# Optimization experiments

Hardware: AMD Instinct MI355X
Metric: run time of the kernel (lower is better)

Reference implementation:

```python
import jax, jax.numpy as jnp
import numpy as np

H, E, V = 1024, 8, 32000
B, S = 2, 2048
RANK, ALPHA = 4, 1.0
LORA_SCALE = ALPHA / RANK
TOP_K = 2
C1, DEC = 4096, 256
CACHE_SIZES = np.array([C1 - i * DEC for i in range(E)])  # [4096,...,2304]
CMAX = int(CACHE_SIZES.max())
H2 = H // 2  # pyramid compression ratio 0.5


def setup_inputs() -> dict:
    key = jax.random.key(0)
    ks = jax.random.split(key, 24)
    n = lambda k, shape, s=1.0: jax.random.normal(k, shape, dtype=jnp.float32) * s
    w = 1.0 / np.sqrt(H)
    inp = {
        "x": n(ks[0], (B, S, H)),
        "query": n(ks[1], (B, S, H)),
        "cache_values": n(ks[2], (E, CMAX, H)),
        "cache_importance": jax.random.uniform(ks[3], (E, CMAX), dtype=jnp.float32),
        "Wr": n(ks[4], (H, E), w),
        "Wexp": n(ks[5], (E, H, H), w),
        "bexp": jnp.zeros((E, H), jnp.float32),
        "Aexp": n(ks[6], (E, H, RANK), w),
        "Bexp": n(ks[7], (E, RANK, H), w),
        "Wq": n(ks[8], (H, H), w),
        "bq": jnp.zeros((H,), jnp.float32),
        "Wk": n(ks[9], (H, H), w),
        "bk": jnp.zeros((H,), jnp.float32),
        "Aq": n(ks[10], (H, RANK), w),
        "Bq": n(ks[11], (RANK, H), w),
        "Ak": n(ks[12], (H, RANK), w),
        "Bk": n(ks[13], (RANK, H), w),
        "Wd": n(ks[14], (H, H2), w),
        "Wu": n(ks[15], (H2, H), 1.0 / np.sqrt(H2)),
        "Av": n(ks[16], (E, H, RANK), w),
        "Bv": n(ks[17], (E, RANK, H), w),
        "Wv": n(ks[18], (H, V), w),
        "bv": jnp.zeros((V,), jnp.float32),
    }
    # compressor weights are per-expert in the original (one per KVCache)
    inp["Wd"] = n(ks[19], (E, H, H2), w)
    inp["Wu"] = n(ks[20], (E, H2, H), 1.0 / np.sqrt(H2))
    return inp


def reference(x, query, cache_values, cache_importance, Wr, Wexp, bexp, Aexp, Bexp,
              Wq, bq, Wk, bk, Aq, Bq, Ak, Bk, Wd, Wu, Av, Bv, Wv, bv):
    # ---- AdaptiveRouter: softmax gate, top-2, renormalize, scatter to dense ----
    gate = jax.nn.softmax(jnp.einsum("bsh,he->bse", x, Wr), axis=-1)       # [B,S,E]
    topv, topi = jax.lax.top_k(gate, TOP_K)                                 # [B,S,K]
    topv = topv / jnp.sum(topv, axis=-1, keepdims=True)
    rw = jnp.sum(jax.nn.one_hot(topi, E, dtype=x.dtype) * topv[..., None], axis=-2)  # [B,S,E]

    # ---- compute_token_importance: LoRA-augmented q/k projections + attention ----
    q = query @ Wq + bq + LORA_SCALE * ((query @ Aq) @ Bq)                  # [B,S,H]
    k = x @ Wk + bk + LORA_SCALE * ((x @ Ak) @ Bk)                          # [B,S,H]
    att = jax.nn.softmax(jnp.einsum("bqh,bkh->bqk", q, k) / np.sqrt(H), axis=-1)
    importance = jnp.sum(att, axis=1)                                       # [B,S] (sum over queries)

    # ---- per-expert KV cache: pyramid compress (down-gelu-up, importance gate) + value LoRA, masked mean ----
    valid = jnp.asarray(np.arange(CMAX)[None, :] < CACHE_SIZES[:, None], x.dtype)  # [E,Cmax]
    h = jax.nn.gelu(jnp.einsum("ech,ehd->ecd", cache_values, Wd))           # [E,Cmax,H2]
    comp = jnp.einsum("ecd,edh->ech", h, Wu) * jax.nn.sigmoid(cache_importance)[..., None]
    comp = comp + LORA_SCALE * jnp.einsum("ech,ehr,erd->ecd", comp, Av, Bv)
    cached = jnp.sum(comp * valid[..., None], axis=1) / jnp.asarray(CACHE_SIZES, x.dtype)[:, None]  # [E,H]

    # ---- dense loop over all LoRA experts (original runs every expert on every token) ----
    eo = jnp.einsum("bsh,ehd->bsed", x, Wexp) + bexp                        # [B,S,E,H]
    eo = eo + LORA_SCALE * jnp.einsum("bsh,ehr,erd->bsed", x, Aexp, Bexp)
    eo = eo + cached[None, None]                                            # broadcast cached values
    expert_output = jnp.einsum("bsed,bse->bsd", eo, rw)                     # routed combine

    logits = expert_output @ Wv + bv                                        # [B,S,V]
    return logits, importance
```

## Files before the change

### kernel.cpp

```cpp
#include <hip/hip_runtime.h>

typedef __bf16 bf16_t;
typedef __bf16 bf16x4 __attribute__((ext_vector_type(4)));
typedef __bf16 bf16x8 __attribute__((ext_vector_type(8)));
typedef float f32x4 __attribute__((ext_vector_type(4)));

#define AS1 __attribute__((address_space(1)))
#define AS3 __attribute__((address_space(3)))
#define BAR() asm volatile("s_barrier" ::: "memory")
#define FENCE() __builtin_amdgcn_sched_barrier(0x10F)

__device__ __forceinline__ void gload_lds16(const void* g, void* l) {
  __builtin_amdgcn_global_load_lds((AS1 void*)g, (AS3 void*)l, 16, 0, 0);
}

__device__ __forceinline__ void stage_tile(const bf16_t* g, int ld, bf16_t* lds, int tid) {
  int w = tid >> 6, lane = tid & 63;
#pragma unroll
  for (int r = 0; r < 2; ++r) {
    int rowbase = r * 64 + w * 16;
    const bf16_t* gp = g + (long)(rowbase + (lane >> 2)) * ld + (lane & 3) * 8;
    bf16_t* lp = lds + rowbase * 32;
    gload_lds16(gp, lp);
  }
}

__device__ __forceinline__ void gemm_core(const bf16_t* A, const bf16_t* Bt, int lda, int ldb,
                                          int K, int rowBase, int colBase,
                                          bf16_t* As, bf16_t* Bs, f32x4 acc[4][4]) {
  int tid = threadIdx.x;
  int lane = tid & 63, w = tid >> 6;
  int wr = w >> 1, wc = w & 1;
  int lr = lane & 15, kg = lane >> 4;
  const bf16_t* Ab = A + (long)rowBase * lda;
  const bf16_t* Bb = Bt + (long)colBase * ldb;
  for (int kt = 0; kt < K; kt += 32) {
    __syncthreads();
    stage_tile(Ab + kt, lda, As, tid);
    stage_tile(Bb + kt, ldb, Bs, tid);
    __syncthreads();
    bf16x8 a[4], b[4];
#pragma unroll
    for (int m = 0; m < 4; ++m)
      a[m] = *(const bf16x8*)&As[(wr * 64 + m * 16 + lr) * 32 + kg * 8];
#pragma unroll
    for (int n = 0; n < 4; ++n)
      b[n] = *(const bf16x8*)&Bs[(wc * 64 + n * 16 + lr) * 32 + kg * 8];
#pragma unroll
    for (int m = 0; m < 4; ++m)
#pragma unroll
      for (int n = 0; n < 4; ++n)
        acc[m][n] = __builtin_amdgcn_mfma_f32_16x16x32_bf16(a[m], b[n], acc[m][n], 0, 0, 0);
  }
}

__device__ __forceinline__ void zero_acc(f32x4 acc[4][4]) {
#pragma unroll
  for (int m = 0; m < 4; ++m)
#pragma unroll
    for (int n = 0; n < 4; ++n)
#pragma unroll
      for (int i = 0; i < 4; ++i) acc[m][n][i] = 0.f;
}

__device__ __forceinline__ void pipe256(const bf16_t* __restrict__ Ag,
                                        const bf16_t* __restrict__ Bg,
                                        int K, int ntk, bf16_t* lds, f32x4 acc[8][4]) {
  int tid = threadIdx.x;
  int lane = tid & 63, w = tid >> 6;
  int wr = w >> 2, wc = w & 3;
  int lr = lane & 15, kg = lane >> 4;
  int colE = ((lane & 7) ^ (lane >> 3)) * 8;
  int r0 = w * 16 + (lane >> 3);

  auto stageA = [&](int t, int h) {
    const bf16_t* g = Ag + (long)(h * 128 + r0) * K + t * 64 + colE;
    bf16_t* l = lds + (t & 1) * 16384 + h * 8192 + w * 1024;
    gload_lds16(g, l);
    gload_lds16(g + (long)8 * K, l + 512);
  };
  auto stageB = [&](int t, int h) {
    const bf16_t* g = Bg + (long)(h * 128 + r0) * K + t * 64 + colE;
    bf16_t* l = lds + 32768 + (t % 3) * 16384 + h * 8192 + w * 1024;
    gload_lds16(g, l);
    gload_lds16(g + (long)8 * K, l + 512);
  };

  stageB(0, 0); stageB(0, 1);
  FENCE();
  stageA(0, 0); stageA(0, 1);
  FENCE();
  if (ntk > 1) { stageB(1, 0); stageB(1, 1); }
  if (ntk > 1) asm volatile("s_waitcnt vmcnt(4)" ::: "memory");
  else         asm volatile("s_waitcnt vmcnt(0)" ::: "memory");
  BAR();

  for (int t = 0; t < ntk; ++t) {
    const bf16_t* Ar = lds + (t & 1) * 16384 + wr * 8192;
    const bf16_t* Br = lds + 32768 + (t % 3) * 16384 + (wc >> 1) * 8192;
    int bRowOff = (wc & 1) * 64;
    if (t + 1 < ntk) { stageA(t + 1, 0); stageA(t + 1, 1); }
    FENCE();
    bf16x8 bfr[4][2];
#pragma unroll
    for (int n = 0; n < 4; ++n) {
      int R = bRowOff + n * 16 + lr;
#pragma unroll
      for (int ks = 0; ks < 2; ++ks)
        bfr[n][ks] = *(const bf16x8*)(Br + R * 64 + ((ks * 4 + kg) ^ (R & 7)) * 8);
    }
#pragma unroll
    for (int p = 0; p < 4; ++p) {
      bf16x8 afr[2][2];
#pragma unroll
      for (int mm = 0; mm < 2; ++mm) {
        int R = p * 32 + mm * 16 + lr;
#pragma unroll
        for (int ks = 0; ks < 2; ++ks)
          afr[mm][ks] = *(const bf16x8*)(Ar + R * 64 + ((ks * 4 + kg) ^ (R & 7)) * 8);
      }
      if (p == 2 && t + 2 < ntk) stageB(t + 2, 0);
      if (p == 3 && t + 2 < ntk) stageB(t + 2, 1);
      __builtin_amdgcn_s_setprio(1);
#pragma unroll
      for (int mm = 0; mm < 2; ++mm)
#pragma unroll
        for (int n = 0; n < 4; ++n)
#pragma unroll
          for (int ks = 0; ks < 2; ++ks)
            acc[p * 2 + mm][n] =
                __builtin_amdgcn_mfma_f32_16x16x32_bf16(afr[mm][ks], bfr[n][ks],
                                                        acc[p * 2 + mm][n], 0, 0, 0);
      __builtin_amdgcn_s_setprio(0);
    }
    if (t + 2 < ntk)      asm volatile("s_waitcnt vmcnt(4)" ::: "memory");
    else if (t + 1 < ntk) asm volatile("s_waitcnt vmcnt(0)" ::: "memory");
    BAR();
  }
}

__global__ __launch_bounds__(256) void k_cast(const float* in, bf16_t* out, long n4) {
  long i = (long)blockIdx.x * 256 + threadIdx.x;
  if (i >= n4) return;
  float4 v = ((const float4*)in)[i];
  bf16_t* o = out + i * 4;
  o[0] = (bf16_t)v.x; o[1] = (bf16_t)v.y; o[2] = (bf16_t)v.z; o[3] = (bf16_t)v.w;
}

__global__ __launch_bounds__(256) void k_cast2(const float* a, const float* b, bf16_t* out) {
  long i = (long)blockIdx.x * 256 + threadIdx.x;
  const float* src = (i < 1048576) ? a : b;
  long j = (i < 1048576) ? i : i - 1048576;
  float4 v = ((const float4*)src)[j];
  bf16_t* o = out + i * 4;
  o[0] = (bf16_t)v.x; o[1] = (bf16_t)v.y; o[2] = (bf16_t)v.z; o[3] = (bf16_t)v.w;
}

__global__ __launch_bounds__(256) void k_prep_wt(const float* W, const float* A, const float* Bm,
                                                 bf16_t* out, int K, int N,
                                                 long wstride, long astride, long bstride, long ostride) {
  __shared__ float tile[64][65];
  int e = blockIdx.z;
  W += (long)e * wstride;
  out += (long)e * ostride;
  if (A) { A += (long)e * astride; Bm += (long)e * bstride; }
  int k0 = blockIdx.x * 64, n0 = blockIdx.y * 64;
  int tid = threadIdx.x;
  int tn = tid & 63, tk = tid >> 6;
#pragma unroll 4
  for (int i = 0; i < 16; ++i) {
    int k = tk + i * 4;
    float v = W[(long)(k0 + k) * N + (n0 + tn)];
    if (A) {
      const float* Ak = A + (long)(k0 + k) * 4;
      const float* Bn = Bm + n0 + tn;
      v += 0.25f * (Ak[0] * Bn[0] + Ak[1] * Bn[(long)N] + Ak[2] * Bn[2L * N] + Ak[3] * Bn[3L * N]);
    }
    tile[k][tn] = v;
  }
  __syncthreads();
#pragma unroll 4
  for (int i = 0; i < 16; ++i) {
    int n = tk + i * 4;
    out[(long)(n0 + n) * K + (k0 + tn)] = (bf16_t)tile[tn][n];
  }
}

__global__ __launch_bounds__(256) void k_router(const float* x, const float* Wr, float* rw) {
  int w = threadIdx.x >> 6, lane = threadIdx.x & 63;
  long tok = (long)blockIdx.x * 4 + w;
  const float* xr = x + tok * 1024;
  float acc[8] = {0.f, 0.f, 0.f, 0.f, 0.f, 0.f, 0.f, 0.f};
  for (int h = lane; h < 1024; h += 64) {
    float xv = xr[h];
    const float* wr8 = Wr + h * 8;
#pragma unroll
    for (int e = 0; e < 8; ++e) acc[e] += xv * wr8[e];
  }
#pragma unroll
  for (int o = 32; o; o >>= 1)
#pragma unroll
    for (int e = 0; e < 8; ++e) acc[e] += __shfl_xor(acc[e], o);
  if (lane == 0) {
    int i1 = 0;
    for (int e = 1; e < 8; ++e) if (acc[e] > acc[i1]) i1 = e;
    int i2 = (i1 == 0) ? 1 : 0;
    for (int e = 0; e < 8; ++e) { if (e == i1) continue; if (acc[e] > acc[i2]) i2 = e; }
    float g2 = expf(acc[i2] - acc[i1]);
    float d = 1.f / (1.f + g2);
    float* dst = rw + tok * 8;
#pragma unroll
    for (int e = 0; e < 8; ++e) dst[e] = (e == i1) ? d : ((e == i2) ? g2 * d : 0.f);
  }
}

__global__ __launch_bounds__(256) void k_sched(const float* rw, int* eidx, float* ewgt, int* tcnt) {
  int e = blockIdx.x, tid = threadIdx.x;
  __shared__ int cnt;
  if (tid == 0) cnt = 0;
  __syncthreads();
  for (int t = tid; t < 4096; t += 256) {
    const float* r = rw + (long)t * 8;
    float wv = r[e];
    if (wv > 0.f) {
      int slot = 0;
      for (int j = 0; j < 8; ++j) if (j < e && r[j] > 0.f) slot = 1;
      int p = atomicAdd(&cnt, 1);
      eidx[e * 4096 + p] = t * 2 + slot;
      ewgt[e * 4096 + p] = wv;
    }
  }
  __syncthreads();
  int c = cnt;
  int padded = (c + 127) & ~127;
  for (int p = c + tid; p < padded; p += 256) eidx[e * 4096 + p] = -1;
  if (tid == 0) tcnt[e] = padded >> 7;
}

__global__ void k_sched2(const int* tcnt, int* desc, int* ntile) {
  if (threadIdx.x == 0 && blockIdx.x == 0) {
    int n = 0;
    for (int e = 0; e < 8; ++e)
      for (int i = 0; i < tcnt[e]; ++i) { desc[n * 2] = e; desc[n * 2 + 1] = i; ++n; }
    *ntile = n;
  }
}

__global__ __launch_bounds__(256) void k_moe128(const bf16_t* x_bf, const bf16_t* wexp_t,
                                                const int* eidx, const float* ewgt,
                                                const int* desc, const int* ntile,
                                                const float* cbc, float* Yp) {
  if ((int)blockIdx.y >= *ntile) return;
  int e = desc[blockIdx.y * 2], ti = desc[blockIdx.y * 2 + 1];
  const int* idx = eidx + e * 4096 + ti * 128;
  const float* wgt = ewgt + e * 4096 + ti * 128;
  __shared__ bf16_t As[4096] __attribute__((aligned(16)));
  __shared__ bf16_t Bs[4096] __attribute__((aligned(16)));
  int tid = threadIdx.x, lane = tid & 63, w = tid >> 6;
  const bf16_t* aP[2];
#pragma unroll
  for (int r = 0; r < 2; ++r) {
    int row = r * 64 + w * 16 + (lane >> 2);
    int v = idx[row];
    int tok = (v < 0) ? 0 : (v >> 1);
    aP[r] = x_bf + (long)tok * 1024 + (lane & 3) * 8;
  }
  const bf16_t* Bb = wexp_t + (long)e * 1048576 + (long)blockIdx.x * 131072;
  int wr = w >> 1, wc = w & 1, lr = lane & 15, kg = lane >> 4;
  f32x4 acc[4][4];
  zero_acc(acc);
  for (int kt = 0; kt < 1024; kt += 32) {
    __syncthreads();
    gload_lds16(aP[0] + kt, As + (w * 16) * 32);
    gload_lds16(aP[1] + kt, As + (64 + w * 16) * 32);
    stage_tile(Bb + kt, 1024, Bs, tid);
    __syncthreads();
    bf16x8 a[4], b[4];
#pragma unroll
    for (int m = 0; m < 4; ++m)
      a[m] = *(const bf16x8*)&As[(wr * 64 + m * 16 + lr) * 32 + kg * 8];
#pragma unroll
    for (int n = 0; n < 4; ++n)
      b[n] = *(const bf16x8*)&Bs[(wc * 64 + n * 16 + lr) * 32 + kg * 8];
#pragma unroll
    for (int m = 0; m < 4; ++m)
#pragma unroll
      for (int n = 0; n < 4; ++n)
        acc[m][n] = __builtin_amdgcn_mfma_f32_16x16x32_bf16(a[m], b[n], acc[m][n], 0, 0, 0);
  }
  const float* cb = cbc + e * 1024 + blockIdx.x * 128;
#pragma unroll
  for (int m = 0; m < 4; ++m)
#pragma unroll
    for (int r = 0; r < 4; ++r) {
      int lrow = wr * 64 + m * 16 + kg * 4 + r;
      int v = idx[lrow];
      if (v < 0) continue;
      int tok = v >> 1, slot = v & 1;
      float wg = wgt[lrow];
      float* op = Yp + ((long)slot * 4096 + tok) * 1024 + blockIdx.x * 128;
#pragma unroll
      for (int n = 0; n < 4; ++n) {
        int gc = wc * 64 + n * 16 + lr;
        op[gc] = wg * (acc[m][n][r] + cb[gc]);
      }
    }
}

__global__ __launch_bounds__(256) void k_combine2(const float* Yp, bf16_t* out) {
  long t = blockIdx.x;
  int d = threadIdx.x * 4;
  f32x4 a = *(const f32x4*)(Yp + t * 1024 + d);
  f32x4 b = *(const f32x4*)(Yp + 4194304L + t * 1024 + d);
  bf16x4 r;
#pragma unroll
  for (int i = 0; i < 4; ++i) r[i] = (bf16_t)(a[i] + b[i]);
  *(bf16x4*)(out + t * 1024 + d) = r;
}

__global__ __launch_bounds__(256) void k_gemm_bias_bf16(const bf16_t* A, long Az,
                                                        const bf16_t* Bt, long Bz,
                                                        const float* bias0, const float* bias1,
                                                        bf16_t* out, long Oz, int K, int ldc) {
  __shared__ bf16_t As[4096] __attribute__((aligned(16)));
  __shared__ bf16_t Bs[4096] __attribute__((aligned(16)));
  int z = blockIdx.z;
  A += (long)z * Az; Bt += (long)z * Bz; out += (long)z * Oz;
  const float* bias = z ? bias1 : bias0;
  int rowBase = blockIdx.x * 128, colBase = blockIdx.y * 128;
  f32x4 acc[4][4];
  zero_acc(acc);
  gemm_core(A, Bt, K, K, K, rowBase, colBase, As, Bs, acc);
  int tid = threadIdx.x, lane = tid & 63, w = tid >> 6;
  int wr = w >> 1, wc = w & 1, lc = lane & 15, kg = lane >> 4;
#pragma unroll
  for (int m = 0; m < 4; ++m)
#pragma unroll
    for (int n = 0; n < 4; ++n)
#pragma unroll
      for (int r = 0; r < 4; ++r) {
        int gr = rowBase + wr * 64 + m * 16 + kg * 4 + r;
        int gc = colBase + wc * 64 + n * 16 + lc;
        out[(long)gr * ldc + gc] = (bf16_t)(acc[m][n][r] + bias[gc]);
      }
}

template <bool NT>
__global__ __launch_bounds__(256) void k_gemm128(
    const bf16_t* __restrict__ A, long Az, const bf16_t* __restrict__ Bt, long Bz,
    const float* __restrict__ bias, float* __restrict__ out, long Oz,
    int mB, int N, int K, float scale) {
  __shared__ bf16_t As[4096] __attribute__((aligned(16)));
  __shared__ bf16_t Bs[4096] __attribute__((aligned(16)));
  __shared__ float fl[32 * 132];
  int tid = threadIdx.x;
  A += (long)blockIdx.y * Az;
  Bt += (long)blockIdx.y * Bz;
  out += (long)blockIdx.y * Oz;
  int per = gridDim.x >> 3;
  int bid = blockIdx.x;
  int swz = (bid & 7) * per + (bid >> 3);
  int rowB = swz % mB, colB = swz / mB;
  int rowBase = rowB << 7, colBase = colB << 7;
  f32x4 acc[4][4];
  zero_acc(acc);
  gemm_core(A, Bt, K, K, K, rowBase, colBase, As, Bs, acc);
  int lane = tid & 63, w = tid >> 6;
  int wr = w >> 1, wc = w & 1, lc = lane & 15, kg = lane >> 4;
  int colq = (tid & 31) * 4;
  f32x4 bb = {0.f, 0.f, 0.f, 0.f};
  if (bias) bb = *(const f32x4*)(bias + colBase + colq);
#pragma unroll
  for (int c = 0; c < 4; ++c) {
    __syncthreads();
    if (wr == (c >> 1)) {
      int m0 = (c & 1) * 2;
#pragma unroll
      for (int mm = 0; mm < 2; ++mm)
#pragma unroll
        for (int n = 0; n < 4; ++n)
#pragma unroll
          for (int r = 0; r < 4; ++r)
            fl[(mm * 16 + kg * 4 + r) * 132 + wc * 64 + n * 16 + lc] = acc[m0 + mm][n][r] * scale;
    }
    __syncthreads();
    long grow = rowBase + c * 32;
#pragma unroll
    for (int q = 0; q < 4; ++q) {
      int idx = q * 256 + tid;
      int row = idx >> 5;
      f32x4 v = *(const f32x4*)&fl[row * 132 + colq];
      v += bb;
      float* op = out + (grow + row) * (long)N + colBase + colq;
      if (NT) __builtin_nontemporal_store(v, (f32x4*)op);
      else *(f32x4*)op = v;
    }
  }
}

template <bool NT>
__global__ __launch_bounds__(512, 2) void k_gemm256(
    const bf16_t* __restrict__ A, long Az, const bf16_t* __restrict__ Bt, long Bz,
    const float* __restrict__ bias, float* __restrict__ out, long Oz,
    int mBlocks, int N, int K, int ntk, float scale) {
  __shared__ bf16_t lds[81920] __attribute__((aligned(16)));
  int tid = threadIdx.x;
  int lane = tid & 63, w = tid >> 6;
  int wr = w >> 2, wc = w & 3;
  int lr = lane & 15, kg = lane >> 4;
  A += (long)blockIdx.y * Az;
  Bt += (long)blockIdx.y * Bz;
  out += (long)blockIdx.y * Oz;
  int per = gridDim.x >> 3;
  int bid = blockIdx.x;
  int swz = (bid & 7) * per + (bid >> 3);
  int rowB = swz % mBlocks, colB = swz / mBlocks;
  long rowBase = (long)rowB << 8, colBase = (long)colB << 8;

  f32x4 acc[8][4];
#pragma unroll
  for (int m = 0; m < 8; ++m)
#pragma unroll
    for (int n = 0; n < 4; ++n)
#pragma unroll
      for (int i = 0; i < 4; ++i) acc[m][n][i] = 0.f;
  pipe256(A + rowBase * K, Bt + colBase * K, K, ntk, lds, acc);

  float* fl = (float*)lds;
  f32x4 bb4 = {0.f, 0.f, 0.f, 0.f};
  if (bias) bb4 = ((const f32x4*)(bias + colBase))[lane];
#pragma unroll
  for (int c = 0; c < 4; ++c) {
    if ((c >> 1) == wr) {
      int mg0 = (c & 1) * 4;
#pragma unroll
      for (int j = 0; j < 4; ++j)
#pragma unroll
        for (int n = 0; n < 4; ++n) {
          int col = wc * 64 + n * 16 + lr;
          int lrow = j * 16 + kg * 4;
#pragma unroll
          for (int rr = 0; rr < 4; ++rr)
            fl[(lrow + rr) * 260 + col] = acc[mg0 + j][n][rr] * scale;
        }
    }
    BAR();
    long grow = rowBase + c * 64;
#pragma unroll
    for (int q = 0; q < 8; ++q) {
      int r = w * 8 + q;
      f32x4 v = *(const f32x4*)&fl[r * 260 + lane * 4];
      v += bb4;
      float* op = out + (grow + r) * (long)N + colBase + lane * 4;
      if (NT) __builtin_nontemporal_store(v, (f32x4*)op);
      else *(f32x4*)op = v;
    }
    BAR();
  }
}

__global__ __launch_bounds__(512, 2) void k_cache256(
    const bf16_t* __restrict__ cache_bf, const bf16_t* __restrict__ wd_t,
    const float* __restrict__ ci, float* __restrict__ partial) {
  __shared__ bf16_t lds[81920] __attribute__((aligned(16)));
  int tid = threadIdx.x;
  int lane = tid & 63, w = tid >> 6;
  int wr = w >> 2, wc = w & 3;
  int lr = lane & 15, kg = lane >> 4;
  int e = blockIdx.y;
  const bf16_t* A = cache_bf + (long)e * 4194304;
  const bf16_t* Bt = wd_t + (long)e * 524288;
  int per = gridDim.x >> 3;
  int bid = blockIdx.x;
  int swz = (bid & 7) * per + (bid >> 3);
  int rowB = swz % 16, colB = swz / 16;
  long rowBase = (long)rowB << 8, colBase = (long)colB << 8;

  f32x4 acc[8][4];
#pragma unroll
  for (int m = 0; m < 8; ++m)
#pragma unroll
    for (int n = 0; n < 4; ++n)
#pragma unroll
      for (int i = 0; i < 4; ++i) acc[m][n][i] = 0.f;
  pipe256(A + rowBase * 1024, Bt + colBase * 1024, 1024, 16, lds, acc);

  float* colsum = (float*)lds;
  if (tid < 256) colsum[tid] = 0.f;
  __syncthreads();
  int csize = 4096 - 256 * e;
  const float* cie = ci + (long)e * 4096;
  float s[4] = {0.f, 0.f, 0.f, 0.f};
#pragma unroll
  for (int mg = 0; mg < 8; ++mg)
#pragma unroll
    for (int rr = 0; rr < 4; ++rr) {
      int row = (int)rowBase + wr * 128 + mg * 16 + kg * 4 + rr;
      float wf = (row < csize) ? 1.f / (1.f + expf(-cie[row])) : 0.f;
#pragma unroll
      for (int n = 0; n < 4; ++n) {
        float xv = acc[mg][n][rr];
        float t = xv + 0.044715f * xv * xv * xv;
        float gl = 0.5f * xv * (1.f + tanhf(0.7978845608028654f * t));
        s[n] += gl * wf;
      }
    }
#pragma unroll
  for (int n = 0; n < 4; ++n)
    atomicAdd(&colsum[wc * 64 + n * 16 + lr], s[n]);
  __syncthreads();
  if (tid < 256)
    partial[((long)e * 16 + rowB) * 512 + colB * 256 + tid] = colsum[tid];
}

__global__ __launch_bounds__(256) void k_wu_mv(const float* partial, const float* Wu, float* pre) {
  int e = blockIdx.x;
  int d = blockIdx.y * 256 + threadIdx.x;
  __shared__ float gs[512];
  for (int j = threadIdx.x; j < 512; j += 256) {
    float s = 0.f;
    for (int mx = 0; mx < 16; ++mx) s += partial[((long)e * 16 + mx) * 512 + j];
    gs[j] = s;
  }
  __syncthreads();
  const float* W = Wu + (long)e * 524288 + d;
  float s = 0.f;
  for (int j = 0; j < 512; ++j) s += gs[j] * W[(long)j * 1024];
  pre[e * 1024 + d] = s;
}

__global__ __launch_bounds__(256) void k_cached_fin(const float* pre, const float* Av,
                                                    const float* Bv, const float* bexp,
                                                    float* cbc) {
  int e = blockIdx.x, tid = threadIdx.x;
  __shared__ float ps[1024];
  __shared__ float tt[4];
  for (int d = tid; d < 1024; d += 256) ps[d] = pre[e * 1024 + d];
  __syncthreads();
  int w = tid >> 6, lane = tid & 63;
  {
    float s = 0.f;
    const float* Ave = Av + e * 4096;
    for (int d = lane; d < 1024; d += 64) s += ps[d] * Ave[d * 4 + w];
#pragma unroll
    for (int o = 32; o; o >>= 1) s += __shfl_xor(s, o);
    if (lane == 0) tt[w] = s;
  }
  __syncthreads();
  float inv = 1.f / (float)(4096 - 256 * e);
  const float* Bve = Bv + e * 4096;
  for (int d = tid; d < 1024; d += 256) {
    float lora = tt[0] * Bve[d] + tt[1] * Bve[1024 + d] + tt[2] * Bve[2048 + d] + tt[3] * Bve[3072 + d];
    cbc[e * 1024 + d] = (ps[d] + 0.25f * lora) * inv + bexp[e * 1024 + d];
  }
}

__global__ __launch_bounds__(256) void k_rowstat(const float* S, float* mrow, float* zinv) {
  long row = blockIdx.x;
  const float* r = S + row * 2048;
  int tid = threadIdx.x;
  float m = -3.4e38f, s = 0.f;
  for (int c = tid; c < 2048; c += 256) {
    float v = r[c];
    if (v > m) { s = s * expf(m - v) + 1.f; m = v; }
    else s += expf(v - m);
  }
#pragma unroll
  for (int o = 32; o; o >>= 1) {
    float mo = __shfl_xor(m, o), so = __shfl_xor(s, o);
    float M = fmaxf(m, mo);
    s = s * expf(m - M) + so * expf(mo - M);
    m = M;
  }
  __shared__ float sm[4], ss[4];
  if ((tid & 63) == 0) { sm[tid >> 6] = m; ss[tid >> 6] = s; }
  __syncthreads();
  if (tid == 0) {
    float M = fmaxf(fmaxf(sm[0], sm[1]), fmaxf(sm[2], sm[3]));
    float S2 = ss[0] * expf(sm[0] - M) + ss[1] * expf(sm[1] - M) +
               ss[2] * expf(sm[2] - M) + ss[3] * expf(sm[3] - M);
    mrow[row] = M;
    zinv[row] = 1.f / S2;
  }
}

__global__ __launch_bounds__(256) void k_imp_part(const float* S, const float* mrow, const float* zinv,
                                                  float* ipart) {
  int k = blockIdx.x * 256 + threadIdx.x;
  int qc = blockIdx.y, b = blockIdx.z;
  const float* Sb = S + (long)b * 4194304;
  const float* mb = mrow + b * 2048;
  const float* zb = zinv + b * 2048;
  float s = 0.f;
  int q0 = qc * 128;
  for (int q = q0; q < q0 + 128; ++q)
    s += expf(Sb[(long)q * 2048 + k] - mb[q]) * zb[q];
  ipart[((long)b * 16 + qc) * 2048 + k] = s;
}

__global__ __launch_bounds__(256) void k_imp_fin(const float* ipart, float* out) {
  int k = blockIdx.x * 256 + threadIdx.x;
  int b = blockIdx.y;
  float s = 0.f;
  for (int qc = 0; qc < 16; ++qc) s += ipart[((long)b * 16 + qc) * 2048 + k];
  out[b * 2048 + k] = s;
}

extern "C" void kernel_launch(void* const* d_in, const int* in_sizes, int n_in,
                              void* d_out, int out_size, void* d_ws, size_t ws_size,
                              hipStream_t stream) {
  (void)in_sizes; (void)n_in; (void)out_size; (void)ws_size;
  const float* x    = (const float*)d_in[0];
  const float* query= (const float*)d_in[1];
  const float* cach = (const float*)d_in[2];
  const float* ci   = (const float*)d_in[3];
  const float* Wr   = (const float*)d_in[4];
  const float* Wexp = (const float*)d_in[5];
  const float* bexp = (const float*)d_in[6];
  const float* Aexp = (const float*)d_in[7];
  const float* Bexp = (const float*)d_in[8];
  const float* Wq   = (const float*)d_in[9];
  const float* bq   = (const float*)d_in[10];
  const float* Wk   = (const float*)d_in[11];
  const float* bk   = (const float*)d_in[12];
  const float* Aq   = (const float*)d_in[13];
  const float* Bq   = (const float*)d_in[14];
  const float* Ak   = (const float*)d_in[15];
  const float* Bk   = (const float*)d_in[16];
  const float* Wd   = (const float*)d_in[17];
  const float* Wu   = (const float*)d_in[18];
  const float* Av   = (const float*)d_in[19];
  const float* Bv   = (const float*)d_in[20];
  const float* Wv   = (const float*)d_in[21];
  const float* bv   = (const float*)d_in[22];
  float* out = (float*)d_out;

  size_t off = 0;
  char* base = (char*)d_ws;
  auto carve = [&](size_t bytes) { char* p = base + off; off = (off + bytes + 255) & ~(size_t)255; return (void*)p; };
  bf16_t* query_bf = (bf16_t*)carve(8388608);
  bf16_t* x_bf     = (bf16_t*)carve(8388608);
  bf16_t* q_bf     = (bf16_t*)carve(8388608);
  bf16_t* k_bf     = (bf16_t*)carve(8388608);
  bf16_t* expert_bf= (bf16_t*)carve(8388608);
  bf16_t* wq_t     = (bf16_t*)carve(2097152);
  bf16_t* wk_t     = (bf16_t*)carve(2097152);
  bf16_t* wd_t     = (bf16_t*)carve(8388608);
  bf16_t* wexp_t   = (bf16_t*)carve(16777216);
  float*  s_att    = (float*)carve(33554432);
  float*  mrow     = (float*)carve(16384);
  float*  zinv     = (float*)carve(16384);
  float*  rw       = (float*)carve(131072);
  float*  partial  = (float*)carve(262144);
  float*  pre      = (float*)carve(32768);
  float*  cbc      = (float*)carve(32768);
  float*  ipart    = (float*)carve(262144);
  int*    eidx     = (int*)carve(131072);
  float*  ewgt     = (float*)carve(131072);
  int*    tcnt     = (int*)carve(256);
  int*    desc     = (int*)carve(1024);
  int*    ntile    = (int*)carve(256);
  void*   uni      = carve(71303168);
  bf16_t* cache_bf = (bf16_t*)uni;
  float*  Yp       = (float*)uni;
  bf16_t* wv_t     = (bf16_t*)uni;

  k_cast2<<<8192, 256, 0, stream>>>(query, x, query_bf);
  k_cast<<<32768, 256, 0, stream>>>(cach, cache_bf, 8388608);
  k_prep_wt<<<dim3(16, 16, 1), 256, 0, stream>>>(Wq, Aq, Bq, wq_t, 1024, 1024, 0, 0, 0, 0);
  k_prep_wt<<<dim3(16, 16, 1), 256, 0, stream>>>(Wk, Ak, Bk, wk_t, 1024, 1024, 0, 0, 0, 0);
  k_prep_wt<<<dim3(16, 8, 8), 256, 0, stream>>>(Wd, nullptr, nullptr, wd_t, 1024, 512, 524288, 0, 0, 524288);
  k_prep_wt<<<dim3(16, 16, 8), 256, 0, stream>>>(Wexp, Aexp, Bexp, wexp_t, 1024, 1024, 1048576, 4096, 4096, 1048576);
  k_router<<<1024, 256, 0, stream>>>(x, Wr, rw);
  k_sched<<<8, 256, 0, stream>>>(rw, eidx, ewgt, tcnt);
  k_sched2<<<1, 64, 0, stream>>>(tcnt, desc, ntile);
  k_gemm_bias_bf16<<<dim3(32, 8, 2), 256, 0, stream>>>(query_bf, 4194304, wq_t, 1048576,
                                                       bq, bk, q_bf, 4194304, 1024, 1024);
  k_gemm128<false><<<dim3(256, 2), 256, 0, stream>>>(q_bf, 2097152, k_bf, 2097152, nullptr,
                                                     s_att, 4194304, 16, 2048, 1024, 0.03125f);
  k_rowstat<<<4096, 256, 0, stream>>>(s_att, mrow, zinv);
  k_imp_part<<<dim3(8, 16, 2), 256, 0, stream>>>(s_att, mrow, zinv, ipart);
  k_imp_fin<<<dim3(8, 2), 256, 0, stream>>>(ipart, out + 131072000L);
  k_cache256<<<dim3(32, 8), 512, 0, stream>>>(cache_bf, wd_t, ci, partial);
  k_wu_mv<<<dim3(8, 4), 256, 0, stream>>>(partial, Wu, pre);
  k_cached_fin<<<8, 256, 0, stream>>>(pre, Av, Bv, bexp, cbc);
  k_moe128<<<dim3(8, 72), 256, 0, stream>>>(x_bf, wexp_t, eidx, ewgt, desc, ntile, cbc, Yp);
  k_combine2<<<4096, 256, 0, stream>>>(Yp, expert_bf);
  k_prep_wt<<<dim3(16, 500, 1), 256, 0, stream>>>(Wv, nullptr, nullptr, wv_t, 1024, 32000, 0, 0, 0, 0);
  k_gemm256<true><<<dim3(2000, 1), 512, 0, stream>>>(expert_bf, 0, wv_t, 0, bv,
                                                     out, 0, 16, 32000, 1024, 16, 1.0f);
}
```

Before: 744.9 us.

## Use 256x128 tiles with smaller LDS pipeline for vocab GEMM; drop sched2 kernel

The final vocab-projection GEMM moves from 256x256 output tiles with a large LDS footprint to 256x128 tiles. It uses a new K=32 pipeline with double-buffered A and triple-buffered B, and launch bounds now allow 4 blocks per CU for higher occupancy and more latency hiding. The single-thread tile-descriptor kernel is removed, and each MoE block derives its expert and tile index from the tile counts directly, saving one launch. The trade-off is less operand reuse per tile and twice as many blocks.

```diff
diff --git a/kernel.cpp b/kernel.cpp
--- a/kernel.cpp
+++ b/kernel.cpp
@@ -134,6 +134,62 @@
       __builtin_amdgcn_s_setprio(0);
     }
     if (t + 2 < ntk)      asm volatile("s_waitcnt vmcnt(4)" ::: "memory");
+    else if (t + 1 < ntk) asm volatile("s_waitcnt vmcnt(0)" ::: "memory");
+    BAR();
+  }
+}
+
+__device__ __forceinline__ void pipe256x128(const bf16_t* __restrict__ Ag,
+                                            const bf16_t* __restrict__ Bg,
+                                            int K, int ntk, bf16_t* lds, f32x4 acc[4][4]) {
+  int tid = threadIdx.x;
+  int lane = tid & 63, w = tid >> 6;
+  int wrr = w >> 1, wcc = w & 1;
+  int lr = lane & 15, kg = lane >> 4;
+  int colE = ((lane & 3) ^ ((lane >> 2) & 3)) * 8;
+  int r0 = w * 16 + (lane >> 2);
+
+  auto stageA = [&](int t, int h) {
+    const bf16_t* g = Ag + (long)(h * 128 + r0) * K + t * 32 + colE;
+    gload_lds16(g, lds + (t & 1) * 8192 + h * 4096 + w * 512);
+  };
+  auto stageB = [&](int t) {
+    const bf16_t* g = Bg + (long)r0 * K + t * 32 + colE;
+    gload_lds16(g, lds + 16384 + (t % 3) * 4096 + w * 512);
+  };
+
+  stageB(0);
+  FENCE();
+  stageA(0, 0); stageA(0, 1);
+  FENCE();
+  if (ntk > 1) stageB(1);
+  if (ntk > 1) asm volatile("s_waitcnt vmcnt(1)" ::: "memory");
+  else         asm volatile("s_waitcnt vmcnt(0)" ::: "memory");
+  BAR();
+
+  for (int t = 0; t < ntk; ++t) {
+    const bf16_t* Ar = lds + (t & 1) * 8192;
+    const bf16_t* Br = lds + 16384 + (t % 3) * 4096;
+    if (t + 1 < ntk) { stageA(t + 1, 0); stageA(t + 1, 1); }
+    FENCE();
+    bf16x8 bfr[4];
+#pragma unroll
+    for (int n = 0; n < 4; ++n) {
+      int R = wcc * 64 + n * 16 + lr;
+      bfr[n] = *(const bf16x8*)(Br + R * 32 + (kg ^ (R & 3)) * 8);
+    }
+#pragma unroll
+    for (int m = 0; m < 4; ++m) {
+      int R = wrr * 64 + m * 16 + lr;
+      bf16x8 afr = *(const bf16x8*)(Ar + R * 32 + (kg ^ (R & 3)) * 8);
+      if (m == 2 && t + 2 < ntk) stageB(t + 2);
+      __builtin_amdgcn_s_setprio(1);
+#pragma unroll
+      for (int n = 0; n < 4; ++n)
+        acc[m][n] = __builtin_amdgcn_mfma_f32_16x16x32_bf16(afr, bfr[n], acc[m][n], 0, 0, 0);
+      __builtin_amdgcn_s_setprio(0);
+    }
+    if (t + 2 < ntk)      asm volatile("s_waitcnt vmcnt(1)" ::: "memory");
     else if (t + 1 < ntk) asm volatile("s_waitcnt vmcnt(0)" ::: "memory");
     BAR();
   }
@@ -237,21 +293,12 @@
   if (tid == 0) tcnt[e] = padded >> 7;
 }
 
-__global__ void k_sched2(const int* tcnt, int* desc, int* ntile) {
-  if (threadIdx.x == 0 && blockIdx.x == 0) {
-    int n = 0;
-    for (int e = 0; e < 8; ++e)
-      for (int i = 0; i < tcnt[e]; ++i) { desc[n * 2] = e; desc[n * 2 + 1] = i; ++n; }
-    *ntile = n;
-  }
-}
-
 __global__ __launch_bounds__(256) void k_moe128(const bf16_t* x_bf, const bf16_t* wexp_t,
                                                 const int* eidx, const float* ewgt,
-                                                const int* desc, const int* ntile,
-                                                const float* cbc, float* Yp) {
-  if ((int)blockIdx.y >= *ntile) return;
-  int e = desc[blockIdx.y * 2], ti = desc[blockIdx.y * 2 + 1];
+                                                const int* tcnt, const float* cbc, float* Yp) {
+  int e = 0, ti = blockIdx.y;
+  while (e < 8 && ti >= tcnt[e]) { ti -= tcnt[e]; ++e; }
+  if (e >= 8) return;
   const int* idx = eidx + e * 4096 + ti * 128;
   const float* wgt = ewgt + e * 4096 + ti * 128;
   __shared__ bf16_t As[4096] __attribute__((aligned(16)));
@@ -399,14 +446,14 @@
 }
 
 template <bool NT>
-__global__ __launch_bounds__(512, 2) void k_gemm256(
+__global__ __launch_bounds__(512, 4) void k_gemm256(
     const bf16_t* __restrict__ A, long Az, const bf16_t* __restrict__ Bt, long Bz,
     const float* __restrict__ bias, float* __restrict__ out, long Oz,
     int mBlocks, int N, int K, int ntk, float scale) {
-  __shared__ bf16_t lds[81920] __attribute__((aligned(16)));
+  __shared__ bf16_t lds[28672] __attribute__((aligned(16)));
   int tid = threadIdx.x;
   int lane = tid & 63, w = tid >> 6;
-  int wr = w >> 2, wc = w & 3;
+  int wrr = w >> 1, wcc = w & 1;
   int lr = lane & 15, kg = lane >> 4;
   A += (long)blockIdx.y * Az;
   Bt += (long)blockIdx.y * Bz;
@@ -415,43 +462,36 @@
   int bid = blockIdx.x;
   int swz = (bid & 7) * per + (bid >> 3);
   int rowB = swz % mBlocks, colB = swz / mBlocks;
-  long rowBase = (long)rowB << 8, colBase = (long)colB << 8;
-
-  f32x4 acc[8][4];
-#pragma unroll
-  for (int m = 0; m < 8; ++m)
-#pragma unroll
-    for (int n = 0; n < 4; ++n)
-#pragma unroll
-      for (int i = 0; i < 4; ++i) acc[m][n][i] = 0.f;
-  pipe256(A + rowBase * K, Bt + colBase * K, K, ntk, lds, acc);
+  long rowBase = (long)rowB << 8, colBase = (long)colB << 7;
+
+  f32x4 acc[4][4];
+  zero_acc(acc);
+  pipe256x128(A + rowBase * K, Bt + colBase * K, K, ntk, lds, acc);
 
   float* fl = (float*)lds;
-  f32x4 bb4 = {0.f, 0.f, 0.f, 0.f};
-  if (bias) bb4 = ((const f32x4*)(bias + colBase))[lane];
+  int colq = (tid & 31) * 4;
+  f32x4 bb = {0.f, 0.f, 0.f, 0.f};
+  if (bias) bb = *(const f32x4*)(bias + colBase + colq);
 #pragma unroll
   for (int c = 0; c < 4; ++c) {
-    if ((c >> 1) == wr) {
-      int mg0 = (c & 1) * 4;
-#pragma unroll
-      for (int j = 0; j < 4; ++j)
-#pragma unroll
-        for (int n = 0; n < 4; ++n) {
-          int col = wc * 64 + n * 16 + lr;
-          int lrow = j * 16 + kg * 4;
+    if (wrr == c) {
+#pragma unroll
+      for (int m = 0; m < 4; ++m)
+#pragma unroll
+        for (int n = 0; n < 4; ++n)
 #pragma unroll
           for (int rr = 0; rr < 4; ++rr)
-            fl[(lrow + rr) * 260 + col] = acc[mg0 + j][n][rr] * scale;
-        }
+            fl[(m * 16 + kg * 4 + rr) * 132 + wcc * 64 + n * 16 + lr] = acc[m][n][rr] * scale;
     }
     BAR();
     long grow = rowBase + c * 64;
 #pragma unroll
-    for (int q = 0; q < 8; ++q) {
-      int r = w * 8 + q;
-      f32x4 v = *(const f32x4*)&fl[r * 260 + lane * 4];
-      v += bb4;
-      float* op = out + (grow + r) * (long)N + colBase + lane * 4;
+    for (int q = 0; q < 4; ++q) {
+      int idx = q * 512 + tid;
+      int row = idx >> 5;
+      f32x4 v = *(const f32x4*)&fl[row * 132 + colq];
+      v += bb;
+      float* op = out + (grow + row) * (long)N + colBase + colq;
       if (NT) __builtin_nontemporal_store(v, (f32x4*)op);
       else *(f32x4*)op = v;
     }
@@ -658,8 +698,6 @@
   int*    eidx     = (int*)carve(131072);
   float*  ewgt     = (float*)carve(131072);
   int*    tcnt     = (int*)carve(256);
-  int*    desc     = (int*)carve(1024);
-  int*    ntile    = (int*)carve(256);
   void*   uni      = carve(71303168);
   bf16_t* cache_bf = (bf16_t*)uni;
   float*  Yp       = (float*)uni;
@@ -673,7 +711,6 @@
   k_prep_wt<<<dim3(16, 16, 8), 256, 0, stream>>>(Wexp, Aexp, Bexp, wexp_t, 1024, 1024, 1048576, 4096, 4096, 1048576);
   k_router<<<1024, 256, 0, stream>>>(x, Wr, rw);
   k_sched<<<8, 256, 0, stream>>>(rw, eidx, ewgt, tcnt);
-  k_sched2<<<1, 64, 0, stream>>>(tcnt, desc, ntile);
   k_gemm_bias_bf16<<<dim3(32, 8, 2), 256, 0, stream>>>(query_bf, 4194304, wq_t, 1048576,
                                                        bq, bk, q_bf, 4194304, 1024, 1024);
   k_gemm128<false><<<dim3(256, 2), 256, 0, stream>>>(q_bf, 2097152, k_bf, 2097152, nullptr,
@@ -684,9 +721,9 @@
   k_cache256<<<dim3(32, 8), 512, 0, stream>>>(cache_bf, wd_t, ci, partial);
   k_wu_mv<<<dim3(8, 4), 256, 0, stream>>>(partial, Wu, pre);
   k_cached_fin<<<8, 256, 0, stream>>>(pre, Av, Bv, bexp, cbc);
-  k_moe128<<<dim3(8, 72), 256, 0, stream>>>(x_bf, wexp_t, eidx, ewgt, desc, ntile, cbc, Yp);
+  k_moe128<<<dim3(8, 72), 256, 0, stream>>>(x_bf, wexp_t, eidx, ewgt, tcnt, cbc, Yp);
   k_combine2<<<4096, 256, 0, stream>>>(Yp, expert_bf);
   k_prep_wt<<<dim3(16, 500, 1), 256, 0, stream>>>(Wv, nullptr, nullptr, wv_t, 1024, 32000, 0, 0, 0, 0);
-  k_gemm256<true><<<dim3(2000, 1), 512, 0, stream>>>(expert_bf, 0, wv_t, 0, bv,
-                                                     out, 0, 16, 32000, 1024, 16, 1.0f);
-}
+  k_gemm256<true><<<dim3(4000, 1), 512, 0, stream>>>(expert_bf, 0, wv_t, 0, bv,
+                                                     out, 0, 16, 32000, 1024, 32, 1.0f);
+}
```

Measured after the change: 768.2 us. 1.03x slower.
